# Kernel tuning notes

Hardware: AMD Instinct MI355X
Metric: run time of the kernel (lower is better)

Reference implementation:

```python
import jax, jax.numpy as jnp
import numpy as np

D_MODEL = 1024
N_LAYERS = 24
K_SUPPRESS = 12
KEEP = N_LAYERS - K_SUPPRESS


def setup_inputs() -> dict:
    key = jax.random.key(0)
    kx, kw = jax.random.split(key)
    B, T = 4, 2000
    x = jax.random.normal(kx, (B, T, N_LAYERS, D_MODEL), dtype=jnp.float32)
    # nn.Linear(d_model, 1, bias=False) weight, stored as a (D,) vector
    w_g = jax.random.normal(kw, (D_MODEL,), dtype=jnp.float32) * (1.0 / np.sqrt(D_MODEL))
    return {"x": x, "w_g": w_g}


def reference(x, w_g):
    """Eval-mode forward of LearnableMask (no noise branch).

    x:   (B, T, N, D)
    w_g: (D,)
    returns (B, T, D)
    """
    # gate scores: (B, T, N)
    scores = jnp.einsum('btnd,d->btn', x, w_g)
    # top-(N-k) indices along layer axis
    _, top_idx = jax.lax.top_k(scores, KEEP)  # (B, T, KEEP)
    # boolean keep-mask via one-hot over the small N axis
    keep_mask = jax.nn.one_hot(top_idx, N_LAYERS, dtype=jnp.bool_).any(axis=-2)  # (B, T, N)
    suppressed = jnp.where(keep_mask, scores, -jnp.inf)
    weights = jax.nn.softmax(suppressed, axis=-1)  # (B, T, N)
    # softmax-weighted layer sum: (B, T, D)
    out = jnp.einsum('btn,btnd->btd', weights, x)
    return out
```

## Files before the change

kernel.cpp:

```cpp
#include <hip/hip_runtime.h>
#include <math.h>

#define NL   24
#define KEEP 12
#define DM   1024
#define BLK  256

__global__ __launch_bounds__(BLK) void lmask_kernel(const float* __restrict__ x,
                                                    const float* __restrict__ wg,
                                                    float* __restrict__ out) {
    const int token = blockIdx.x;
    const int tid   = threadIdx.x;
    const int lane  = tid & 63;
    const int wave  = tid >> 6;
    const int d0    = tid * 4;

    const float* xt = x + (size_t)token * (NL * DM);

    __shared__ float swave[4][NL];
    __shared__ float s_w[NL];

    const float4 wv = *reinterpret_cast<const float4*>(wg + d0);

    float4 xr[NL];
    float  part[NL];
#pragma unroll
    for (int n = 0; n < NL; ++n) {
        xr[n] = *reinterpret_cast<const float4*>(xt + n * DM + d0);
        part[n] = xr[n].x * wv.x + xr[n].y * wv.y + xr[n].z * wv.z + xr[n].w * wv.w;
    }

#pragma unroll
    for (int n = 0; n < NL; ++n) {
        float v = part[n];
        v += __shfl_xor(v, 1);
        v += __shfl_xor(v, 2);
        v += __shfl_xor(v, 4);
        v += __shfl_xor(v, 8);
        v += __shfl_xor(v, 16);
        v += __shfl_xor(v, 32);
        part[n] = v;
    }
    if (lane == 0) {
#pragma unroll
        for (int n = 0; n < NL; ++n) swave[wave][n] = part[n];
    }
    __syncthreads();

    if (tid < 64) {
        float sc_own = -INFINITY;
        if (lane < NL)
            sc_own = swave[0][lane] + swave[1][lane] + swave[2][lane] + swave[3][lane];

        int rank = 0;
#pragma unroll
        for (int m = 0; m < NL; ++m) {
            float scm = swave[0][m] + swave[1][m] + swave[2][m] + swave[3][m];
            rank += ((scm > sc_own) || (scm == sc_own && m < lane)) ? 1 : 0;
        }
        const bool keep = (lane < NL) && (rank < KEEP);

        float val = keep ? sc_own : -INFINITY;
        float mx = val;
        mx = fmaxf(mx, __shfl_xor(mx, 1));
        mx = fmaxf(mx, __shfl_xor(mx, 2));
        mx = fmaxf(mx, __shfl_xor(mx, 4));
        mx = fmaxf(mx, __shfl_xor(mx, 8));
        mx = fmaxf(mx, __shfl_xor(mx, 16));
        mx = fmaxf(mx, __shfl_xor(mx, 32));

        float e = keep ? __expf(sc_own - mx) : 0.0f;
        float s = e;
        s += __shfl_xor(s, 1);
        s += __shfl_xor(s, 2);
        s += __shfl_xor(s, 4);
        s += __shfl_xor(s, 8);
        s += __shfl_xor(s, 16);
        s += __shfl_xor(s, 32);

        if (lane < NL) s_w[lane] = e / s;
    }
    __syncthreads();

    float4 acc = make_float4(0.f, 0.f, 0.f, 0.f);
#pragma unroll
    for (int n = 0; n < NL; ++n) {
        const float w = s_w[n];
        acc.x = fmaf(w, xr[n].x, acc.x);
        acc.y = fmaf(w, xr[n].y, acc.y);
        acc.z = fmaf(w, xr[n].z, acc.z);
        acc.w = fmaf(w, xr[n].w, acc.w);
    }
    reinterpret_cast<float4*>(out + (size_t)token * DM)[tid] = acc;
}

extern "C" void kernel_launch(void* const* d_in, const int* in_sizes, int n_in,
                              void* d_out, int out_size, void* d_ws, size_t ws_size,
                              hipStream_t stream) {
    const float* x  = (const float*)d_in[0];
    const float* wg = (const float*)d_in[1];
    float* out      = (float*)d_out;
    const int tokens = in_sizes[0] / (NL * DM);
    lmask_kernel<<<tokens, BLK, 0, stream>>>(x, wg, out);
}
```

Baseline: 151.3 us.

## Split layer axis across four thread groups with 1024-thread blocks

Each token block now uses 1024 threads, with four groups of 256 each loading 6 of the 24 layers, so each thread holds far fewer float4 registers. Every wave computes the gate scores, top-k rank and softmax redundantly using shuffles, which removes one barrier and the shared weight array. The partial weighted sums are then reduced through shared memory. The aim is higher occupancy and more memory parallelism for this bandwidth-bound kernel, at the cost of duplicated softmax work and an extra shared-memory reduction.

```diff
diff --git a/kernel.cpp b/kernel.cpp
--- a/kernel.cpp
+++ b/kernel.cpp
@@ -1,97 +1,110 @@
 #include <hip/hip_runtime.h>
 #include <math.h>
 
-#define NL   24
-#define KEEP 12
-#define DM   1024
-#define BLK  256
+#define NL    24
+#define KEEP  12
+#define DM    1024
+#define BLK   1024
+#define LPT   6
 
-__global__ __launch_bounds__(BLK) void lmask_kernel(const float* __restrict__ x,
-                                                    const float* __restrict__ wg,
-                                                    float* __restrict__ out) {
+__global__ __launch_bounds__(BLK, 8) void lmask_kernel(const float* __restrict__ x,
+                                                       const float* __restrict__ wg,
+                                                       float* __restrict__ out) {
     const int token = blockIdx.x;
     const int tid   = threadIdx.x;
     const int lane  = tid & 63;
     const int wave  = tid >> 6;
-    const int d0    = tid * 4;
+    const int q     = tid >> 8;
+    const int colg  = tid & 255;
+    const int d0    = colg * 4;
+    const int nbase = q * LPT;
 
     const float* xt = x + (size_t)token * (NL * DM);
 
-    __shared__ float swave[4][NL];
-    __shared__ float s_w[NL];
+    __shared__ float  swave[16][LPT];
+    __shared__ float4 pacc[3][256];
 
     const float4 wv = *reinterpret_cast<const float4*>(wg + d0);
 
-    float4 xr[NL];
-    float  part[NL];
+    float4 xr[LPT];
+    float  part[LPT];
 #pragma unroll
-    for (int n = 0; n < NL; ++n) {
-        xr[n] = *reinterpret_cast<const float4*>(xt + n * DM + d0);
-        part[n] = xr[n].x * wv.x + xr[n].y * wv.y + xr[n].z * wv.z + xr[n].w * wv.w;
+    for (int j = 0; j < LPT; ++j) {
+        xr[j]   = *reinterpret_cast<const float4*>(xt + (nbase + j) * DM + d0);
+        part[j] = xr[j].x * wv.x + xr[j].y * wv.y + xr[j].z * wv.z + xr[j].w * wv.w;
     }
 
 #pragma unroll
-    for (int n = 0; n < NL; ++n) {
-        float v = part[n];
+    for (int j = 0; j < LPT; ++j) {
+        float v = part[j];
         v += __shfl_xor(v, 1);
         v += __shfl_xor(v, 2);
         v += __shfl_xor(v, 4);
         v += __shfl_xor(v, 8);
         v += __shfl_xor(v, 16);
         v += __shfl_xor(v, 32);
-        part[n] = v;
+        part[j] = v;
     }
     if (lane == 0) {
 #pragma unroll
-        for (int n = 0; n < NL; ++n) swave[wave][n] = part[n];
+        for (int j = 0; j < LPT; ++j) swave[wave][j] = part[j];
     }
     __syncthreads();
 
-    if (tid < 64) {
-        float sc_own = -INFINITY;
-        if (lane < NL)
-            sc_own = swave[0][lane] + swave[1][lane] + swave[2][lane] + swave[3][lane];
+    float sc = -INFINITY;
+    if (lane < NL) {
+        const int qn = lane / LPT, jn = lane % LPT;
+        sc = swave[4*qn + 0][jn] + swave[4*qn + 1][jn]
+           + swave[4*qn + 2][jn] + swave[4*qn + 3][jn];
+    }
+    int rank = 0;
+#pragma unroll
+    for (int m = 0; m < NL; ++m) {
+        const float sm = __shfl(sc, m);
+        rank += ((sm > sc) || (sm == sc && m < lane)) ? 1 : 0;
+    }
+    const bool keep = (lane < NL) && (rank < KEEP);
 
-        int rank = 0;
-#pragma unroll
-        for (int m = 0; m < NL; ++m) {
-            float scm = swave[0][m] + swave[1][m] + swave[2][m] + swave[3][m];
-            rank += ((scm > sc_own) || (scm == sc_own && m < lane)) ? 1 : 0;
-        }
-        const bool keep = (lane < NL) && (rank < KEEP);
+    float val = keep ? sc : -INFINITY;
+    float mx = val;
+    mx = fmaxf(mx, __shfl_xor(mx, 1));
+    mx = fmaxf(mx, __shfl_xor(mx, 2));
+    mx = fmaxf(mx, __shfl_xor(mx, 4));
+    mx = fmaxf(mx, __shfl_xor(mx, 8));
+    mx = fmaxf(mx, __shfl_xor(mx, 16));
 
-        float val = keep ? sc_own : -INFINITY;
-        float mx = val;
-        mx = fmaxf(mx, __shfl_xor(mx, 1));
-        mx = fmaxf(mx, __shfl_xor(mx, 2));
-        mx = fmaxf(mx, __shfl_xor(mx, 4));
-        mx = fmaxf(mx, __shfl_xor(mx, 8));
-        mx = fmaxf(mx, __shfl_xor(mx, 16));
-        mx = fmaxf(mx, __shfl_xor(mx, 32));
-
-        float e = keep ? __expf(sc_own - mx) : 0.0f;
-        float s = e;
-        s += __shfl_xor(s, 1);
-        s += __shfl_xor(s, 2);
-        s += __shfl_xor(s, 4);
-        s += __shfl_xor(s, 8);
-        s += __shfl_xor(s, 16);
-        s += __shfl_xor(s, 32);
-
-        if (lane < NL) s_w[lane] = e / s;
-    }
-    __syncthreads();
+    float e = keep ? __expf(sc - mx) : 0.0f;
+    float s = e;
+    s += __shfl_xor(s, 1);
+    s += __shfl_xor(s, 2);
+    s += __shfl_xor(s, 4);
+    s += __shfl_xor(s, 8);
+    s += __shfl_xor(s, 16);
+    const float wfin = e / s;
 
     float4 acc = make_float4(0.f, 0.f, 0.f, 0.f);
 #pragma unroll
-    for (int n = 0; n < NL; ++n) {
-        const float w = s_w[n];
-        acc.x = fmaf(w, xr[n].x, acc.x);
-        acc.y = fmaf(w, xr[n].y, acc.y);
-        acc.z = fmaf(w, xr[n].z, acc.z);
-        acc.w = fmaf(w, xr[n].w, acc.w);
+    for (int j = 0; j < LPT; ++j) {
+        const float w = __shfl(wfin, nbase + j);
+        acc.x = fmaf(w, xr[j].x, acc.x);
+        acc.y = fmaf(w, xr[j].y, acc.y);
+        acc.z = fmaf(w, xr[j].z, acc.z);
+        acc.w = fmaf(w, xr[j].w, acc.w);
     }
-    reinterpret_cast<float4*>(out + (size_t)token * DM)[tid] = acc;
+
+    if (q > 0) pacc[q - 1][colg] = acc;
+    __syncthreads();
+
+    if (q == 0) {
+        const float4 a = pacc[0][colg];
+        const float4 b = pacc[1][colg];
+        const float4 c = pacc[2][colg];
+        acc.x += a.x + b.x + c.x;
+        acc.y += a.y + b.y + c.y;
+        acc.z += a.z + b.z + c.z;
+        acc.w += a.w + b.w + c.w;
+        reinterpret_cast<float4*>(out + (size_t)token * DM)[colg] = acc;
+    }
 }
 
 extern "C" void kernel_launch(void* const* d_in, const int* in_sizes, int n_in,
```

New measurement: 147.0 us. 1.03x faster.
